# Kernel tuning notes

Measured on AMD Instinct MI355X. Metric: run time of the kernel, lower is better.

## Reference

```python
import jax, jax.numpy as jnp
import numpy as np

N_NODES = 50000
N_EDGES = 800000
N_GRAPHS = 512
IN_DIM, HID_DIM, EMB_DIM = 128, 256, 128
EPS = 1e-5


def setup_inputs() -> dict:
    key = jax.random.key(0)
    ks = jax.random.split(key, 12)
    x = jax.random.normal(ks[0], (N_NODES, IN_DIM), dtype=jnp.float32)
    edge_index = jax.random.randint(ks[1], (2, N_EDGES), 0, N_NODES, dtype=jnp.int32)
    batch = jnp.sort(jax.random.randint(ks[2], (N_NODES,), 0, N_GRAPHS, dtype=jnp.int32))
    s1 = 1.0 / np.sqrt(IN_DIM)
    s2 = 1.0 / np.sqrt(HID_DIM)
    return {
        "x": x,
        "edge_index": edge_index,
        "batch": batch,
        "W1": jax.random.uniform(ks[3], (IN_DIM, HID_DIM), jnp.float32, -s1, s1),
        "b1": jnp.zeros((HID_DIM,), jnp.float32),
        "gamma1": jnp.ones((HID_DIM,), jnp.float32),
        "beta1": jnp.zeros((HID_DIM,), jnp.float32),
        "W2": jax.random.uniform(ks[4], (HID_DIM, EMB_DIM), jnp.float32, -s2, s2),
        "b2": jnp.zeros((EMB_DIM,), jnp.float32),
        "gamma2": jnp.ones((EMB_DIM,), jnp.float32),
        "beta2": jnp.zeros((EMB_DIM,), jnp.float32),
    }


def _gcn_conv(x, W, b, src, dst, n_nodes):
    # PyG GCNConv: h = xW; aggregate with sym-normalized adjacency incl. self-loops; + bias
    h = x @ W  # [N, D]
    ones = jnp.ones(src.shape[0], dtype=h.dtype)
    deg = jax.ops.segment_sum(ones, dst, num_segments=n_nodes) + 1.0  # self-loop
    dinv = jax.lax.rsqrt(deg)
    norm = dinv[src] * dinv[dst]  # [E]
    msg = h[src] * norm[:, None]  # gather + scale  [E, D]
    agg = jax.ops.segment_sum(msg, dst, num_segments=n_nodes)
    agg = agg + h * (1.0 / deg)[:, None]  # self-loop contribution (norm = 1/deg)
    return agg + b


def _batchnorm(h, gamma, beta):
    mean = jnp.mean(h, axis=0)
    var = jnp.mean(jnp.square(h - mean), axis=0)  # biased, training mode
    return gamma * (h - mean) * jax.lax.rsqrt(var + EPS) + beta


def reference(x, edge_index, batch, W1, b1, gamma1, beta1, W2, b2, gamma2, beta2):
    src, dst = edge_index[0], edge_index[1]
    n = x.shape[0]
    h = _gcn_conv(x, W1, b1, src, dst, n)
    h = _batchnorm(jax.nn.relu(h), gamma1, beta1)
    h = _gcn_conv(h, W2, b2, src, dst, n)
    h = _batchnorm(jax.nn.relu(h), gamma2, beta2)
    return jax.ops.segment_max(h, batch, num_segments=N_GRAPHS)
```

## Files before the change

### kernel.cpp

```cpp
#include <hip/hip_runtime.h>
#include <math.h>

#define N_NODES 50000
#define N_EDGES 800000
#define N_GRAPHS 512
#define IN_DIM 128
#define HID_DIM 256
#define EMB_DIM 128
#define EPS 1e-5f
#define ELLW 64
#define NV4 (N_EDGES / 4)
#define NB 196
#define CAP 8192
#define PA_BLOCKS 512
#define CPB ((NV4 + PA_BLOCKS - 1) / PA_BLOCKS)
#define F2B_N (N_NODES * IN_DIM / 4)
#define F2B_BLOCKS ((F2B_N + 255) / 256)
#define TW1_BLOCKS ((HID_DIM * IN_DIM + 255) / 256)
#define NSLOTS 128
#define GSLOTS 128

typedef __attribute__((ext_vector_type(8))) short bf16x8;
typedef __attribute__((ext_vector_type(4))) float f32x4;
typedef __attribute__((ext_vector_type(4))) int i32x4;
typedef __attribute__((ext_vector_type(4))) unsigned short u16x4;

static __device__ __forceinline__ unsigned short f2b(float f) {
    unsigned u = __float_as_uint(f);
    return (unsigned short)((u + 0x7fffu + ((u >> 16) & 1u)) >> 16);
}
static __device__ __forceinline__ float dinv_of(int d) {
    return rsqrtf((float)(min(d, ELLW) + 1));
}

__global__ void __launch_bounds__(256) scatter_convert(const int* __restrict__ src,
                                                       const int* __restrict__ dst,
                                                       int* __restrict__ gcur,
                                                       int* __restrict__ bucketbuf,
                                                       const float* __restrict__ x,
                                                       unsigned short* __restrict__ xbf,
                                                       const float* __restrict__ W1,
                                                       unsigned short* __restrict__ W1t) {
    int b = blockIdx.x;
    if (b < PA_BLOCKS) {
        __shared__ int hcnt[NB], hbase[NB], loff[NB];
        int t = threadIdx.x;
        for (int j = t; j < NB; j += 256) { hcnt[j] = 0; loff[j] = 0; }
        __syncthreads();
        int base = b * CPB;
        int i_end = min(base + CPB, NV4);
        const i32x4* dst4 = (const i32x4*)dst;
        const i32x4* src4 = (const i32x4*)src;
        int i0 = base + t, i1 = base + 256 + t;
        bool val0 = i0 < i_end, val1 = i1 < i_end;
        i32x4 d0 = {0, 0, 0, 0}, s0 = {0, 0, 0, 0};
        i32x4 d1 = {0, 0, 0, 0}, s1 = {0, 0, 0, 0};
        if (val0) {
            d0 = __builtin_nontemporal_load(&dst4[i0]);
            s0 = __builtin_nontemporal_load(&src4[i0]);
        }
        if (val1) {
            d1 = __builtin_nontemporal_load(&dst4[i1]);
            s1 = __builtin_nontemporal_load(&src4[i1]);
        }
        if (val0) {
#pragma unroll
            for (int e = 0; e < 4; ++e) atomicAdd(&hcnt[d0[e] >> 8], 1);
        }
        if (val1) {
#pragma unroll
            for (int e = 0; e < 4; ++e) atomicAdd(&hcnt[d1[e] >> 8], 1);
        }
        __syncthreads();
        for (int j = t; j < NB; j += 256) {
            int c = hcnt[j];
            if (c) hbase[j] = atomicAdd(&gcur[j], c);
        }
        __syncthreads();
        if (val0) {
#pragma unroll
            for (int e = 0; e < 4; ++e) {
                int d = d0[e], bk = d >> 8;
                int o = atomicAdd(&loff[bk], 1);
                int idx = hbase[bk] + o;
                if (idx < CAP) bucketbuf[bk * CAP + idx] = ((d & 255) << 16) | s0[e];
            }
        }
        if (val1) {
#pragma unroll
            for (int e = 0; e < 4; ++e) {
                int d = d1[e], bk = d >> 8;
                int o = atomicAdd(&loff[bk], 1);
                int idx = hbase[bk] + o;
                if (idx < CAP) bucketbuf[bk * CAP + idx] = ((d & 255) << 16) | s1[e];
            }
        }
    } else if (b < PA_BLOCKS + F2B_BLOCKS) {
        int i = (b - PA_BLOCKS) * 256 + threadIdx.x;
        if (i < F2B_N) {
            f32x4 v = __builtin_nontemporal_load(&((const f32x4*)x)[i]);
            u16x4 o;
            o[0] = f2b(v[0]); o[1] = f2b(v[1]); o[2] = f2b(v[2]); o[3] = f2b(v[3]);
            __builtin_nontemporal_store(o, &((u16x4*)xbf)[i]);
        }
    } else {
        int j = (b - PA_BLOCKS - F2B_BLOCKS) * 256 + threadIdx.x;
        if (j < HID_DIM * IN_DIM) {
            int n = j >> 7;
            int k = j & 127;
            W1t[j] = f2b(W1[k * HID_DIM + n]);
        }
    }
}

__global__ void __launch_bounds__(256) build_ell(const int* __restrict__ gcur,
                                                 const int* __restrict__ bucketbuf,
                                                 int* __restrict__ fill,
                                                 int* __restrict__ col) {
    __shared__ unsigned short lcol[256 * ELLW];
    __shared__ int lfill[256];
    int b = blockIdx.x;
    int t = threadIdx.x;
    lfill[t] = 0;
    __syncthreads();
    int n = min(gcur[b], CAP);
    const int* buf = bucketbuf + b * CAP;
    for (int i = t; i < n; i += 256) {
        int p = buf[i];
        int dl = p >> 16;
        int pos = atomicAdd(&lfill[dl], 1);
        if (pos < ELLW) lcol[(dl << 6) + pos] = (unsigned short)(p & 0xFFFF);
    }
    __syncthreads();
    int v = (b << 8) + t;
    if (v < N_NODES) fill[v] = lfill[t];
    for (int idx4 = t; idx4 < 256 * (ELLW / 4); idx4 += 256) {
        int row = idx4 >> 4;
        int vv = (b << 8) + row;
        if (vv < N_NODES) {
            int c0 = (idx4 & 15) << 2;
            u16x4 w = *(const u16x4*)&lcol[(row << 6) + c0];
            int4 o4 = make_int4(w[0], w[1], w[2], w[3]);
            *(int4*)&col[((size_t)vv << 6) + c0] = o4;
        }
    }
}

static __device__ __forceinline__ void acc8(float* acc, uint4 r, float w) {
    const unsigned* u = (const unsigned*)&r;
#pragma unroll
    for (int k = 0; k < 4; ++k) {
        float lo = __uint_as_float((u[k] & 0xFFFFu) << 16);
        float hi = __uint_as_float(u[k] & 0xFFFF0000u);
        acc[2 * k]     += w * lo;
        acc[2 * k + 1] += w * hi;
    }
}

template <bool RELU, bool OUT_BF, bool BIAS, bool STATS>
__global__ void __launch_bounds__(256) aggw_kernel(const unsigned short* __restrict__ h,
                                                   const int* __restrict__ deg,
                                                   const int* __restrict__ col,
                                                   const float* __restrict__ bias,
                                                   void* __restrict__ y,
                                                   float* __restrict__ sumP,
                                                   float* __restrict__ sqP) {
    __shared__ float sv[STATS ? 4 : 1][STATS ? 128 : 1];
    int tid = threadIdx.x;
    int lane = tid & 63;
    int wid = tid >> 6;
    int v = blockIdx.x * 4 + wid;
    int g = lane >> 4;
    int p = lane & 15;

    int dcl = min(deg[v], ELLW);
    int cv = col[(v << 6) + lane];
    int u_l = (lane < dcl) ? cv : v;
    float w_l = (lane < dcl) ? dinv_of(deg[u_l]) : 0.f;

    uint4 selfr = make_uint4(0u, 0u, 0u, 0u);
    if (g == 0) selfr = *(const uint4*)(h + (size_t)v * 128 + p * 8);

    float acc[8] = {};
    for (int base = 0; base < dcl; base += 16) {
        int i0 = base + g, i1 = base + 4 + g, i2 = base + 8 + g, i3 = base + 12 + g;
        int u0 = __shfl(u_l, i0, 64), u1 = __shfl(u_l, i1, 64);
        int u2 = __shfl(u_l, i2, 64), u3 = __shfl(u_l, i3, 64);
        float w0 = __shfl(w_l, i0, 64), w1 = __shfl(w_l, i1, 64);
        float w2 = __shfl(w_l, i2, 64), w3 = __shfl(w_l, i3, 64);
        uint4 d0 = *(const uint4*)(h + (size_t)u0 * 128 + p * 8);
        uint4 d1 = *(const uint4*)(h + (size_t)u1 * 128 + p * 8);
        uint4 d2 = *(const uint4*)(h + (size_t)u2 * 128 + p * 8);
        uint4 d3 = *(const uint4*)(h + (size_t)u3 * 128 + p * 8);
        acc8(acc, d0, w0);
        acc8(acc, d1, w1);
        acc8(acc, d2, w2);
        acc8(acc, d3, w3);
    }

#pragma unroll
    for (int k = 0; k < 8; ++k) {
        float a = acc[k];
        a += __shfl_xor(a, 16, 64);
        a += __shfl_xor(a, 32, 64);
        acc[k] = a;
    }

    if (g == 0) {
        const unsigned* su = (const unsigned*)&selfr;
        float dv = rsqrtf((float)(dcl + 1));
        float dv2 = dv * dv;
        float o[8];
#pragma unroll
        for (int k = 0; k < 4; ++k) {
            float lo = __uint_as_float((su[k] & 0xFFFFu) << 16);
            float hi = __uint_as_float(su[k] & 0xFFFF0000u);
            o[2 * k]     = dv * acc[2 * k]     + lo * dv2;
            o[2 * k + 1] = dv * acc[2 * k + 1] + hi * dv2;
        }
        if (BIAS) {
            float4 bv0 = *(const float4*)&bias[p * 8];
            float4 bv1 = *(const float4*)&bias[p * 8 + 4];
            o[0] += bv0.x; o[1] += bv0.y; o[2] += bv0.z; o[3] += bv0.w;
            o[4] += bv1.x; o[5] += bv1.y; o[6] += bv1.z; o[7] += bv1.w;
        }
        if (RELU) {
#pragma unroll
            for (int k = 0; k < 8; ++k) o[k] = fmaxf(o[k], 0.f);
        }
        if (OUT_BF) {
            uint4 packed;
            unsigned* pu = (unsigned*)&packed;
#pragma unroll
            for (int k = 0; k < 4; ++k)
                pu[k] = (unsigned)f2b(o[2 * k]) | ((unsigned)f2b(o[2 * k + 1]) << 16);
            *(uint4*)((unsigned short*)y + (size_t)v * 128 + p * 8) = packed;
        } else {
            float* yf = (float*)y + (size_t)v * 128 + p * 8;
            *(float4*)yf = make_float4(o[0], o[1], o[2], o[3]);
            *(float4*)(yf + 4) = make_float4(o[4], o[5], o[6], o[7]);
        }
        if (STATS) {
#pragma unroll
            for (int k = 0; k < 8; ++k) sv[wid][p * 8 + k] = o[k];
        }
    }

    if (STATS) {
        __syncthreads();
        if (tid < 128) {
            float s = 0.f, q = 0.f;
#pragma unroll
            for (int w = 0; w < 4; ++w) {
                float val = sv[w][tid];
                s += val;
                q += val * val;
            }
            int slot = blockIdx.x & (NSLOTS - 1);
            atomicAdd(&sumP[slot * 128 + tid], s);
            atomicAdd(&sqP[slot * 128 + tid], q);
        }
    }
}

template <bool RELU, bool STATS>
__global__ void __launch_bounds__(256) mfma_gemm_kernel(const unsigned short* __restrict__ A,
                                                        const unsigned short* __restrict__ Bt,
                                                        const float* __restrict__ bias,
                                                        unsigned short* __restrict__ C,
                                                        float* __restrict__ sums,
                                                        float* __restrict__ sumsqs,
                                                        int M, int N, int K) {
    const int LDT = 40;
    __shared__ unsigned short As[64 * LDT];
    __shared__ unsigned short Bs[64 * LDT];
    int tid = threadIdx.x;
    int bm = blockIdx.x * 64;
    int bn = blockIdx.y * 64;
    int lr = tid >> 2;
    int lc = (tid & 3) * 8;
    int lane = tid & 63;
    int w = tid >> 6;
    int wr = (w >> 1) * 32, wc = (w & 1) * 32;
    int l15 = lane & 15, q = lane >> 4;

    f32x4 acc[2][2] = {};
    bool arow_ok = (bm + lr) < M;
    const unsigned short* Aptr = A + (size_t)(bm + lr) * K + lc;
    const unsigned short* Bptr = Bt + (size_t)(bn + lr) * K + lc;

    uint4 av = arow_ok ? *(const uint4*)(Aptr) : make_uint4(0u, 0u, 0u, 0u);
    uint4 bv = *(const uint4*)(Bptr);

    for (int k0 = 0; k0 < K; k0 += 32) {
        *(uint4*)&As[lr * LDT + lc] = av;
        *(uint4*)&Bs[lr * LDT + lc] = bv;
        __syncthreads();
        if (k0 + 32 < K) {
            av = arow_ok ? *(const uint4*)(Aptr + k0 + 32) : make_uint4(0u, 0u, 0u, 0u);
            bv = *(const uint4*)(Bptr + k0 + 32);
        }
        bf16x8 a0 = *(const bf16x8*)&As[(wr + 0 + l15) * LDT + q * 8];
        bf16x8 a1 = *(const bf16x8*)&As[(wr + 16 + l15) * LDT + q * 8];
        bf16x8 b0 = *(const bf16x8*)&Bs[(wc + 0 + l15) * LDT + q * 8];
        bf16x8 b1 = *(const bf16x8*)&Bs[(wc + 16 + l15) * LDT + q * 8];
        acc[0][0] = __builtin_amdgcn_mfma_f32_16x16x32_bf16(a0, b0, acc[0][0], 0, 0, 0);
        acc[0][1] = __builtin_amdgcn_mfma_f32_16x16x32_bf16(a0, b1, acc[0][1], 0, 0, 0);
        acc[1][0] = __builtin_amdgcn_mfma_f32_16x16x32_bf16(a1, b0, acc[1][0], 0, 0, 0);
        acc[1][1] = __builtin_amdgcn_mfma_f32_16x16x32_bf16(a1, b1, acc[1][1], 0, 0, 0);
        __syncthreads();
    }

    float scol[2] = {0.f, 0.f};
    float qcol[2] = {0.f, 0.f};
#pragma unroll
    for (int mi = 0; mi < 2; ++mi)
#pragma unroll
        for (int ni = 0; ni < 2; ++ni) {
            int colc = bn + wc + ni * 16 + l15;
            float bv2 = bias ? bias[colc] : 0.f;
#pragma unroll
            for (int r = 0; r < 4; ++r) {
                int row = bm + wr + mi * 16 + q * 4 + r;
                if (row < M) {
                    float vv = acc[mi][ni][r] + bv2;
                    if (RELU) vv = fmaxf(vv, 0.f);
                    C[(size_t)row * N + colc] = f2b(vv);
                    if (STATS) { scol[ni] += vv; qcol[ni] += vv * vv; }
                }
            }
        }

    if (STATS) {
        __shared__ float sred[4][2][16];
        __shared__ float qred[4][2][16];
#pragma unroll
        for (int ni = 0; ni < 2; ++ni) {
            float s = scol[ni], qq = qcol[ni];
            s += __shfl_xor(s, 16, 64);
            s += __shfl_xor(s, 32, 64);
            qq += __shfl_xor(qq, 16, 64);
            qq += __shfl_xor(qq, 32, 64);
            if (lane < 16) { sred[w][ni][l15] = s; qred[w][ni][l15] = qq; }
        }
        __syncthreads();
        if (tid < 64) {
            int par = (tid >> 5) & 1;
            int ni = (tid >> 4) & 1;
            int l = tid & 15;
            int slot = blockIdx.x & (GSLOTS - 1);
            atomicAdd(&sums[slot * HID_DIM + bn + tid],
                      sred[par][ni][l] + sred[par + 2][ni][l]);
            atomicAdd(&sumsqs[slot * HID_DIM + bn + tid],
                      qred[par][ni][l] + qred[par + 2][ni][l]);
        }
    }
}

__global__ void __launch_bounds__(256) prep2_kernel(const float* __restrict__ sum1P,
                                                    const float* __restrict__ sumsq1P,
                                                    const float* __restrict__ gamma1,
                                                    const float* __restrict__ beta1,
                                                    const float* __restrict__ W2,
                                                    unsigned short* __restrict__ W2pt,
                                                    float* __restrict__ bc2) {
    __shared__ float a1s[HID_DIM], s1s[HID_DIM];
    __shared__ float bp[16][17];
    int t = threadIdx.x;
    {
        float s = 0.f, q = 0.f;
#pragma unroll 8
        for (int j = 0; j < GSLOTS; ++j) {
            s += sum1P[j * HID_DIM + t];
            q += sumsq1P[j * HID_DIM + t];
        }
        float m = s * (1.f / N_NODES);
        float var = q * (1.f / N_NODES) - m * m;
        float a = gamma1[t] * rsqrtf(var + EPS);
        a1s[t] = a;
        s1s[t] = beta1[t] - m * a;
    }
    __syncthreads();
    int row = blockIdx.x * 16 + (t & 15);
    int ks = t >> 4;
    float bacc = 0.f;
    unsigned short wloc[16];
#pragma unroll
    for (int j = 0; j < 16; ++j) {
        int k = ks * 16 + j;
        float wv = W2[k * EMB_DIM + row];
        wloc[j] = f2b(a1s[k] * wv);
        bacc += s1s[k] * wv;
    }
    *(uint4*)&W2pt[(size_t)row * HID_DIM + ks * 16]     = *(uint4*)&wloc[0];
    *(uint4*)&W2pt[(size_t)row * HID_DIM + ks * 16 + 8] = *(uint4*)&wloc[8];
    bp[t & 15][ks] = bacc;
    __syncthreads();
    if (t < 16) {
        float s = 0.f;
#pragma unroll
        for (int g = 0; g < 16; ++g) s += bp[t][g];
        bc2[blockIdx.x * 16 + t] = s;
    }
}

__global__ void __launch_bounds__(128) segmax_kernel(const float* __restrict__ y,
                                                     const float* __restrict__ sumP,
                                                     const float* __restrict__ sqP,
                                                     const float* __restrict__ gamma2,
                                                     const float* __restrict__ beta2,
                                                     const int* __restrict__ batch,
                                                     float* __restrict__ out) {
    __shared__ int sh[2];
    int g = blockIdx.x;
    int c = threadIdx.x;
    float s2 = 0.f, q2 = 0.f;
#pragma unroll 8
    for (int j = 0; j < NSLOTS; ++j) {
        s2 += sumP[j * 128 + c];
        q2 += sqP[j * 128 + c];
    }
    float mch = s2 * (1.f / N_NODES);
    float var = q2 * (1.f / N_NODES) - mch * mch;
    float ac = gamma2[c] * rsqrtf(var + EPS);
    float sc = beta2[c] - mch * ac;
    if (threadIdx.x == 0) {
        int lo = 0, hi = N_NODES;
        while (lo < hi) { int mid = (lo + hi) >> 1; if (batch[mid] < g) lo = mid + 1; else hi = mid; }
        sh[0] = lo;
        hi = N_NODES;
        while (lo < hi) { int mid = (lo + hi) >> 1; if (batch[mid] < g + 1) lo = mid + 1; else hi = mid; }
        sh[1] = lo;
    }
    __syncthreads();
    int beg = sh[0], end = sh[1];
    float m = -INFINITY;
    for (int v = beg; v < end; ++v) {
        m = fmaxf(m, fmaf(ac, y[(size_t)v * EMB_DIM + c], sc));
    }
    out[(size_t)g * EMB_DIM + c] = m;
}

extern "C" void kernel_launch(void* const* d_in, const int* in_sizes, int n_in,
                              void* d_out, int out_size, void* d_ws, size_t ws_size,
                              hipStream_t stream) {
    const float* x      = (const float*)d_in[0];
    const int*   ei     = (const int*)d_in[1];
    const int*   batch  = (const int*)d_in[2];
    const float* W1     = (const float*)d_in[3];
    const float* b1     = (const float*)d_in[4];
    const float* gamma1 = (const float*)d_in[5];
    const float* beta1  = (const float*)d_in[6];
    const float* W2     = (const float*)d_in[7];
    const float* b2     = (const float*)d_in[8];
    const float* gamma2 = (const float*)d_in[9];
    const float* beta2  = (const float*)d_in[10];
    float* out = (float*)d_out;

    char* ws = (char*)d_ws;
    size_t off = 0;
    auto alloc = [&](size_t bytes) -> char* {
        char* p = ws + off;
        off = (off + bytes + 255) & ~(size_t)255;
        return p;
    };
    int*   gcur    = (int*)alloc((size_t)NB * 4);
    float* gsumP   = (float*)alloc((size_t)GSLOTS * HID_DIM * 4);
    float* gsqP    = (float*)alloc((size_t)GSLOTS * HID_DIM * 4);
    float* sumP    = (float*)alloc((size_t)NSLOTS * 128 * 4);
    float* sqP     = (float*)alloc((size_t)NSLOTS * 128 * 4);
    size_t zbytes = off;
    int*   fill   = (int*)alloc((size_t)N_NODES * 4);
    int*   bucketbuf = (int*)alloc((size_t)NB * CAP * 4);
    int*   col    = (int*)alloc((size_t)N_NODES * ELLW * 4);
    float* bc2    = (float*)alloc((size_t)EMB_DIM * 4);
    unsigned short* W1t  = (unsigned short*)alloc((size_t)HID_DIM * IN_DIM * 2);
    unsigned short* W2pt = (unsigned short*)alloc((size_t)HID_DIM * EMB_DIM * 2);
    unsigned short* xbf  = (unsigned short*)alloc((size_t)N_NODES * IN_DIM * 2);
    unsigned short* axbf = (unsigned short*)alloc((size_t)N_NODES * IN_DIM * 2);
    unsigned short* y1bf = (unsigned short*)alloc((size_t)N_NODES * HID_DIM * 2);
    unsigned short* gbf  = (unsigned short*)alloc((size_t)N_NODES * EMB_DIM * 2);
    float* y2 = (float*)xbf;
    (void)ws_size; (void)in_sizes; (void)n_in; (void)out_size;

    const int* src  = ei;
    const int* dstp = ei + N_EDGES;

    hipMemsetAsync(ws, 0, zbytes, stream);

    scatter_convert<<<PA_BLOCKS + F2B_BLOCKS + TW1_BLOCKS, 256, 0, stream>>>(
        src, dstp, gcur, bucketbuf, x, xbf, W1, W1t);
    build_ell<<<NB, 256, 0, stream>>>(gcur, bucketbuf, fill, col);

    aggw_kernel<false, true, false, false><<<N_NODES / 4, 256, 0, stream>>>(
        xbf, fill, col, nullptr, axbf, nullptr, nullptr);
    dim3 g1((N_NODES + 63) / 64, HID_DIM / 64);
    mfma_gemm_kernel<true, true><<<g1, 256, 0, stream>>>(axbf, W1t, b1, y1bf,
                                                         gsumP, gsqP,
                                                         N_NODES, HID_DIM, IN_DIM);

    prep2_kernel<<<8, 256, 0, stream>>>(gsumP, gsqP, gamma1, beta1, W2, W2pt, bc2);

    dim3 g2((N_NODES + 63) / 64, EMB_DIM / 64);
    mfma_gemm_kernel<false, false><<<g2, 256, 0, stream>>>(y1bf, W2pt, bc2, gbf,
                                                           nullptr, nullptr,
                                                           N_NODES, EMB_DIM, HID_DIM);
    aggw_kernel<true, false, true, true><<<N_NODES / 4, 256, 0, stream>>>(
        gbf, fill, col, b2, y2, sumP, sqP);

    segmax_kernel<<<N_GRAPHS, 128, 0, stream>>>(y2, sumP, sqP,
                                                gamma2, beta2, batch, out);
}
```

Measured before the change: 262.4 us.

## Map each node to a 16-lane group instead of a full wavefront in aggregation

The GCN aggregation kernel now processes 16 nodes per block, one per 16-lane group, instead of 4 nodes per block with one node per wavefront. Each group loads its own neighbor indices and weights and walks the edges serially. This removes the cross-group shuffle reduction and the idle lanes in the epilogue, and raises useful work per wave. In exchange, nodes with different degrees in the same wave now diverge, and each node's edges are no longer spread over four groups, so fewer loads are in flight per node.

```diff
diff --git a/kernel.cpp b/kernel.cpp
--- a/kernel.cpp
+++ b/kernel.cpp
@@ -165,48 +165,49 @@
                                                    void* __restrict__ y,
                                                    float* __restrict__ sumP,
                                                    float* __restrict__ sqP) {
-    __shared__ float sv[STATS ? 4 : 1][STATS ? 128 : 1];
+    __shared__ float sv[STATS ? 16 : 1][STATS ? 128 : 1];
     int tid = threadIdx.x;
     int lane = tid & 63;
-    int wid = tid >> 6;
-    int v = blockIdx.x * 4 + wid;
-    int g = lane >> 4;
+    int grpw = lane >> 4;
     int p = lane & 15;
+    int grp = tid >> 4;
+    int v = blockIdx.x * 16 + grp;
 
     int dcl = min(deg[v], ELLW);
-    int cv = col[(v << 6) + lane];
-    int u_l = (lane < dcl) ? cv : v;
-    float w_l = (lane < dcl) ? dinv_of(deg[u_l]) : 0.f;
-
-    uint4 selfr = make_uint4(0u, 0u, 0u, 0u);
-    if (g == 0) selfr = *(const uint4*)(h + (size_t)v * 128 + p * 8);
+    uint4 selfr = *(const uint4*)(h + (size_t)v * 128 + p * 8);
 
     float acc[8] = {};
-    for (int base = 0; base < dcl; base += 16) {
-        int i0 = base + g, i1 = base + 4 + g, i2 = base + 8 + g, i3 = base + 12 + g;
-        int u0 = __shfl(u_l, i0, 64), u1 = __shfl(u_l, i1, 64);
-        int u2 = __shfl(u_l, i2, 64), u3 = __shfl(u_l, i3, 64);
-        float w0 = __shfl(w_l, i0, 64), w1 = __shfl(w_l, i1, 64);
-        float w2 = __shfl(w_l, i2, 64), w3 = __shfl(w_l, i3, 64);
-        uint4 d0 = *(const uint4*)(h + (size_t)u0 * 128 + p * 8);
-        uint4 d1 = *(const uint4*)(h + (size_t)u1 * 128 + p * 8);
-        uint4 d2 = *(const uint4*)(h + (size_t)u2 * 128 + p * 8);
-        uint4 d3 = *(const uint4*)(h + (size_t)u3 * 128 + p * 8);
-        acc8(acc, d0, w0);
-        acc8(acc, d1, w1);
-        acc8(acc, d2, w2);
-        acc8(acc, d3, w3);
-    }
-
-#pragma unroll
-    for (int k = 0; k < 8; ++k) {
-        float a = acc[k];
-        a += __shfl_xor(a, 16, 64);
-        a += __shfl_xor(a, 32, 64);
-        acc[k] = a;
-    }
-
-    if (g == 0) {
+    int sl = grpw << 4;
+#pragma unroll 4
+    for (int sel = 0; sel < 4; ++sel) {
+        int base = sel * 16;
+        if (base >= dcl) break;
+        int idx = base + p;
+        int cidx = min(idx, dcl - 1);
+        int u_l = col[(v << 6) + cidx];
+        float w_l = (idx < dcl) ? dinv_of(deg[u_l]) : 0.f;
+        int n = min(16, dcl - base);
+        for (int e0 = 0; e0 < n; e0 += 4) {
+            int u0 = __shfl(u_l, sl + e0, 64);
+            int u1 = __shfl(u_l, sl + e0 + 1, 64);
+            int u2 = __shfl(u_l, sl + e0 + 2, 64);
+            int u3 = __shfl(u_l, sl + e0 + 3, 64);
+            float w0 = __shfl(w_l, sl + e0, 64);
+            float w1 = __shfl(w_l, sl + e0 + 1, 64);
+            float w2 = __shfl(w_l, sl + e0 + 2, 64);
+            float w3 = __shfl(w_l, sl + e0 + 3, 64);
+            uint4 d0 = *(const uint4*)(h + (size_t)u0 * 128 + p * 8);
+            uint4 d1 = *(const uint4*)(h + (size_t)u1 * 128 + p * 8);
+            uint4 d2 = *(const uint4*)(h + (size_t)u2 * 128 + p * 8);
+            uint4 d3 = *(const uint4*)(h + (size_t)u3 * 128 + p * 8);
+            acc8(acc, d0, w0);
+            acc8(acc, d1, w1);
+            acc8(acc, d2, w2);
+            acc8(acc, d3, w3);
+        }
+    }
+
+    {
         const unsigned* su = (const unsigned*)&selfr;
         float dv = rsqrtf((float)(dcl + 1));
         float dv2 = dv * dv;
@@ -242,7 +243,7 @@
         }
         if (STATS) {
 #pragma unroll
-            for (int k = 0; k < 8; ++k) sv[wid][p * 8 + k] = o[k];
+            for (int k = 0; k < 8; ++k) sv[grp][p * 8 + k] = o[k];
         }
     }
 
@@ -251,8 +252,8 @@
         if (tid < 128) {
             float s = 0.f, q = 0.f;
 #pragma unroll
-            for (int w = 0; w < 4; ++w) {
-                float val = sv[w][tid];
+            for (int r = 0; r < 16; ++r) {
+                float val = sv[r][tid];
                 s += val;
                 q += val * val;
             }
@@ -492,7 +493,7 @@
         src, dstp, gcur, bucketbuf, x, xbf, W1, W1t);
     build_ell<<<NB, 256, 0, stream>>>(gcur, bucketbuf, fill, col);
 
-    aggw_kernel<false, true, false, false><<<N_NODES / 4, 256, 0, stream>>>(
+    aggw_kernel<false, true, false, false><<<N_NODES / 16, 256, 0, stream>>>(
         xbf, fill, col, nullptr, axbf, nullptr, nullptr);
     dim3 g1((N_NODES + 63) / 64, HID_DIM / 64);
     mfma_gemm_kernel<true, true><<<g1, 256, 0, stream>>>(axbf, W1t, b1, y1bf,
@@ -505,7 +506,7 @@
     mfma_gemm_kernel<false, false><<<g2, 256, 0, stream>>>(y1bf, W2pt, bc2, gbf,
                                                            nullptr, nullptr,
                                                            N_NODES, EMB_DIM, HID_DIM);
-    aggw_kernel<true, false, true, true><<<N_NODES / 4, 256, 0, stream>>>(
+    aggw_kernel<true, false, true, true><<<N_NODES / 16, 256, 0, stream>>>(
         gbf, fill, col, b2, y2, sumP, sqP);
 
     segmax_kernel<<<N_GRAPHS, 128, 0, stream>>>(y2, sumP, sqP,
```

Measured after the change: 259.1 us, median of 2. About the same (-1.2%).
